# Optimization experiments

Measured on AMD Instinct MI355X. Metric: run time of the kernel, lower is better.

Reference implementation:

```python
import jax, jax.numpy as jnp
import numpy as np


def _grid_sample_bilinear(img, grid):
    # img: [N, C, H, W]; grid: [N, Ho, Wo, 2] (x,y) in [-1,1]
    # matches torch.nn.functional.grid_sample(mode='bilinear', padding_mode='zeros', align_corners=False)
    N, C, H, W = img.shape
    Ho, Wo = grid.shape[1], grid.shape[2]
    ix = (grid[..., 0] + 1.0) * (W * 0.5) - 0.5  # unnormalize, align_corners=False
    iy = (grid[..., 1] + 1.0) * (H * 0.5) - 0.5
    x0 = jnp.floor(ix)
    y0 = jnp.floor(iy)
    x1 = x0 + 1.0
    y1 = y0 + 1.0
    wx1 = ix - x0
    wx0 = 1.0 - wx1
    wy1 = iy - y0
    wy0 = 1.0 - wy1
    img_flat = img.reshape(N, C, H * W)

    def corner(xf, yf, w):
        valid = (xf >= 0) & (xf <= W - 1) & (yf >= 0) & (yf <= H - 1)
        xi = jnp.clip(xf.astype(jnp.int32), 0, W - 1)
        yi = jnp.clip(yf.astype(jnp.int32), 0, H - 1)
        idx = (yi * W + xi).reshape(N, 1, Ho * Wo)
        vals = jnp.take_along_axis(img_flat, idx, axis=2)  # [N, C, Ho*Wo]
        wv = (w * valid.astype(img.dtype)).reshape(N, 1, Ho * Wo)
        return vals * wv

    out = (corner(x0, y0, wx0 * wy0) + corner(x1, y0, wx1 * wy0)
           + corner(x0, y1, wx0 * wy1) + corner(x1, y1, wx1 * wy1))
    return out.reshape(N, C, Ho, Wo)


def setup_inputs() -> dict:
    key = jax.random.key(0)
    k1, k2 = jax.random.split(key)
    B, L, C, H, W = 2, 24, 16, 64, 64
    flows = jax.random.normal(k1, (B, L, 2, H, W), dtype=jnp.float32) * 0.01
    images = jax.random.normal(k2, (B, L, C, H, W), dtype=jnp.float32)
    return {"flows": flows, "images": images}


def reference(flows, images):
    B, L, _, H, W = flows.shape
    C = images.shape[2]
    dtype = flows.dtype
    cum_flows = jnp.cumsum(flows.astype(jnp.float32), axis=1).astype(dtype)  # [B,L,2,H,W]
    k_idx, t_idx = np.triu_indices(L)  # all pairs k <= t, N_pairs = L(L+1)/2
    N_pairs = k_idx.size
    # relative flow from frame k to frame t for every pair
    rel = (cum_flows[:, t_idx] - cum_flows[:, k_idx])  # [B, N_pairs, 2, H, W]
    rel = rel.reshape(B * N_pairs, 2, H, W).transpose(0, 2, 3, 1)  # [BN, H, W, 2]
    # pixel-center base grid (align_corners=False convention)
    gy = jnp.linspace(-1.0 + 1.0 / H, 1.0 - 1.0 / H, H, dtype=dtype)
    gx = jnp.linspace(-1.0 + 1.0 / W, 1.0 - 1.0 / W, W, dtype=dtype)
    base = jnp.stack(jnp.meshgrid(gx, gy, indexing='xy'), axis=-1)  # [H, W, 2] (x,y)
    grid = base[None] + rel
    # wrap x coordinate into [-1, 1)
    grid = grid.at[..., 0].set(jnp.remainder(grid[..., 0] + 1.0, 2.0) - 1.0)
    flat_images = images[:, k_idx].reshape(B * N_pairs, C, H, W)
    warped = _grid_sample_bilinear(flat_images, grid)  # [BN, C, H, W]
    targets = (np.arange(B)[:, None] * L + t_idx[None, :]).reshape(-1)
    out = jax.ops.segment_sum(warped, jnp.asarray(targets), num_segments=B * L)
    return out.reshape(B, L, C, H, W)
```

## Files before the change

kernel.cpp:

```cpp
#include <hip/hip_runtime.h>


#define BB 2
#define LL 24
#define CC 16
#define HH 64
#define WW 64
#define HW (HH * WW)

__device__ __forceinline__ void bilin_coords(
    float gxv0, float gyv,
    int& i00, int& i10, int& i01, int& i11,
    float& w00, float& w10, float& w01, float& w11)
{
    const float v = gxv0 + 1.0f;
    float r = v - 2.0f * truncf(v * 0.5f);
    r = (r < 0.0f) ? (r + 2.0f) : r;
    const float gxv = r - 1.0f;

    const float ix = (gxv + 1.0f) * 32.0f - 0.5f;
    const float iy = (gyv + 1.0f) * 32.0f - 0.5f;

    const float x0f = floorf(ix);
    const float y0f = floorf(iy);
    const float x1f = x0f + 1.0f;
    const float y1f = y0f + 1.0f;

    const float wx1 = ix - x0f, wx0 = 1.0f - wx1;
    const float wy1 = iy - y0f, wy0 = 1.0f - wy1;

    const bool vx0 = (x0f >= 0.0f) && (x0f <= 63.0f);
    const bool vx1 = (x1f >= 0.0f) && (x1f <= 63.0f);
    const bool vy0 = (y0f >= 0.0f) && (y0f <= 63.0f);
    const bool vy1 = (y1f >= 0.0f) && (y1f <= 63.0f);

    const int x0 = min(max((int)x0f, 0), WW - 1);
    const int x1 = min(max((int)x1f, 0), WW - 1);
    const int y0 = min(max((int)y0f, 0), HH - 1);
    const int y1 = min(max((int)y1f, 0), HH - 1);

    w00 = (vx0 && vy0) ? (wx0 * wy0) : 0.0f;
    w10 = (vx1 && vy0) ? (wx1 * wy0) : 0.0f;
    w01 = (vx0 && vy1) ? (wx0 * wy1) : 0.0f;
    w11 = (vx1 && vy1) ? (wx1 * wy1) : 0.0f;

    i00 = y0 * WW + x0;
    i10 = y0 * WW + x1;
    i01 = y1 * WW + x0;
    i11 = y1 * WW + x1;
}

__global__ __launch_bounds__(64) void transpose_kernel(
    const float* __restrict__ img, float* __restrict__ imgT)
{
    const int bid = blockIdx.x;
    const int y = bid % HH;
    const int l = (bid / HH) % LL;
    const int b = bid / (HH * LL);
    const int x = threadIdx.x;

    const float* src = img + ((size_t)(b * LL + l) * CC) * HW + y * WW + x;
    float v[CC];
#pragma unroll
    for (int c = 0; c < CC; ++c) v[c] = src[(size_t)c * HW];

    float* dst = imgT + ((size_t)(b * LL + l) * HW + y * WW + x) * CC;
#pragma unroll
    for (int c = 0; c < CC; c += 4)
        *(float4*)(dst + c) = make_float4(v[c], v[c + 1], v[c + 2], v[c + 3]);
}

__global__ __launch_bounds__(256) void gsps_main(
    const float* __restrict__ flows,
    const float* __restrict__ imgT,
    float* __restrict__ out)
{
    const int bid = blockIdx.x;
    const int t = (LL - 1) - (bid % LL);
    const int y = (bid / LL) % HH;
    const int b = bid / (LL * HH);
    const int x = threadIdx.x & 63;
    const int wave = threadIdx.x >> 6;
    const int cw = wave * 4;

    const float gx = -0.984375f + (float)x * 0.03125f;
    const float gy = -0.984375f + (float)y * 0.03125f;
    const int pix = y * WW + x;
    const float* fb = flows + (size_t)b * LL * 2 * HW + pix;

    float ctx = 0.0f, cty = 0.0f;
    for (int i = 0; i <= t; ++i) {
        ctx += fb[(size_t)(i * 2) * HW];
        cty += fb[(size_t)(i * 2 + 1) * HW];
    }

    float4 acc = make_float4(0.0f, 0.0f, 0.0f, 0.0f);
    float cx = 0.0f, cy = 0.0f;
    float fxk = fb[0];
    float fyk = fb[HW];

    const char* ibase = (const char*)(imgT + (size_t)b * LL * HW * CC) + cw * 4;

    for (int k = 0; k <= t; ++k) {
        cx += fxk; cy += fyk;

        if (k < t) {
            fxk = fb[(size_t)((k + 1) * 2) * HW];
            fyk = fb[(size_t)((k + 1) * 2 + 1) * HW];
        }

        int i00, i10, i01, i11;
        float w00, w10, w01, w11;
        bilin_coords(gx + (ctx - cx), gy + (cty - cy), i00, i10, i01, i11, w00, w10, w01, w11);

        const char* p = ibase + (size_t)k * (HW * CC * 4);
        const float4 v00 = *(const float4*)(p + (size_t)i00 * 64);
        const float4 v10 = *(const float4*)(p + (size_t)i10 * 64);
        const float4 v01 = *(const float4*)(p + (size_t)i01 * 64);
        const float4 v11 = *(const float4*)(p + (size_t)i11 * 64);

        acc.x += v00.x * w00 + v10.x * w10 + v01.x * w01 + v11.x * w11;
        acc.y += v00.y * w00 + v10.y * w10 + v01.y * w01 + v11.y * w11;
        acc.z += v00.z * w00 + v10.z * w10 + v01.z * w01 + v11.z * w11;
        acc.w += v00.w * w00 + v10.w * w10 + v01.w * w01 + v11.w * w11;
    }

    float* o = out + ((size_t)(b * LL + t) * CC + cw) * HW + pix;
    o[0]      = acc.x;
    o[HW]     = acc.y;
    o[2 * HW] = acc.z;
    o[3 * HW] = acc.w;
}

__global__ __launch_bounds__(256) void gsps_direct(
    const float* __restrict__ flows,
    const float* __restrict__ images,
    float* __restrict__ out)
{
    const int bid = blockIdx.x;
    const int t = (LL - 1) - (bid % LL);
    const int y = (bid / LL) % HH;
    const int b = bid / (LL * HH);
    const int x = threadIdx.x & 63;
    const int wave = threadIdx.x >> 6;
    const int cw = wave * 4;

    const float gx = -0.984375f + (float)x * 0.03125f;
    const float gy = -0.984375f + (float)y * 0.03125f;
    const int pix = y * WW + x;
    const float* fb = flows + (size_t)b * LL * 2 * HW + pix;

    float ctx = 0.0f, cty = 0.0f;
    for (int i = 0; i <= t; ++i) {
        ctx += fb[(size_t)(i * 2) * HW];
        cty += fb[(size_t)(i * 2 + 1) * HW];
    }

    float acc[4] = {0.0f, 0.0f, 0.0f, 0.0f};
    float cx = 0.0f, cy = 0.0f;
    float fxk = fb[0];
    float fyk = fb[HW];

    for (int k = 0; k <= t; ++k) {
        cx += fxk; cy += fyk;
        if (k < t) {
            fxk = fb[(size_t)((k + 1) * 2) * HW];
            fyk = fb[(size_t)((k + 1) * 2 + 1) * HW];
        }

        int i00, i10, i01, i11;
        float w00, w10, w01, w11;
        bilin_coords(gx + (ctx - cx), gy + (cty - cy), i00, i10, i01, i11, w00, w10, w01, w11);

        const float* img = images + (((size_t)(b * LL + k) * CC) + cw) * HW;
#pragma unroll
        for (int c = 0; c < 4; ++c) {
            const float* pc = img + (size_t)c * HW;
            acc[c] += pc[i00] * w00 + pc[i10] * w10 + pc[i01] * w01 + pc[i11] * w11;
        }
    }

    float* o = out + ((size_t)(b * LL + t) * CC + cw) * HW + pix;
#pragma unroll
    for (int c = 0; c < 4; ++c) o[(size_t)c * HW] = acc[c];
}

extern "C" void kernel_launch(void* const* d_in, const int* in_sizes, int n_in,
                              void* d_out, int out_size, void* d_ws, size_t ws_size,
                              hipStream_t stream) {
    const float* flows  = (const float*)d_in[0];
    const float* images = (const float*)d_in[1];
    float* out = (float*)d_out;

    const size_t needT = (size_t)BB * LL * CC * HW * sizeof(float);
    const int nblk = BB * LL * HH;

    if (ws_size >= needT) {
        float* imgT = (float*)d_ws;
        transpose_kernel<<<nblk, 64, 0, stream>>>(images, imgT);
        gsps_main<<<nblk, 256, 0, stream>>>(flows, imgT, out);
    } else {
        gsps_direct<<<nblk, 256, 0, stream>>>(flows, images, out);
    }
}
```

Before: 169.5 us.

## Compute all 16 channels per thread and interleave row-block order

```diff
diff --git a/kernel.cpp b/kernel.cpp
--- a/kernel.cpp
+++ b/kernel.cpp
@@ -70,9 +70,83 @@
         *(float4*)(dst + c) = make_float4(v[c], v[c + 1], v[c + 2], v[c + 3]);
 }
 
-__global__ __launch_bounds__(256) void gsps_main(
+__global__ __launch_bounds__(64) void gsps_main(
     const float* __restrict__ flows,
     const float* __restrict__ imgT,
+    float* __restrict__ out)
+{
+    const int bid = blockIdx.x;
+    const int y_lo = bid & 7;
+    const int r1 = bid >> 3;
+    const int t = (LL - 1) - (r1 % LL);
+    const int r2 = r1 / LL;
+    const int y = ((r2 & 7) << 3) | y_lo;
+    const int b = r2 >> 3;
+    const int x = threadIdx.x;
+
+    const float gx = -0.984375f + (float)x * 0.03125f;
+    const float gy = -0.984375f + (float)y * 0.03125f;
+    const int pix = y * WW + x;
+    const float* fb = flows + (size_t)b * LL * 2 * HW + pix;
+
+    float ctx = 0.0f, cty = 0.0f;
+    for (int i = 0; i <= t; ++i) {
+        ctx += fb[(size_t)(2 * i) * HW];
+        cty += fb[(size_t)(2 * i + 1) * HW];
+    }
+
+    float acc[CC];
+#pragma unroll
+    for (int c = 0; c < CC; ++c) acc[c] = 0.0f;
+
+    const char* pb = (const char*)imgT + (size_t)b * LL * HW * 64;
+    float cx = 0.0f, cy = 0.0f;
+    float fkx = fb[0], fky = fb[HW];
+
+    for (int k = 0; k <= t; ++k) {
+        cx += fkx; cy += fky;
+        if (k < t) {
+            fkx = fb[(size_t)(2 * (k + 1)) * HW];
+            fky = fb[(size_t)(2 * (k + 1) + 1) * HW];
+        }
+
+        int i00, i10, i01, i11;
+        float w00, w10, w01, w11;
+        bilin_coords(gx + (ctx - cx), gy + (cty - cy), i00, i10, i01, i11, w00, w10, w01, w11);
+
+        const char* plane = pb + (size_t)k * (HW * 64);
+        const float4* r00 = (const float4*)(plane + (size_t)i00 * 64);
+        const float4* r10 = (const float4*)(plane + (size_t)i10 * 64);
+        const float4* r01 = (const float4*)(plane + (size_t)i01 * 64);
+        const float4* r11 = (const float4*)(plane + (size_t)i11 * 64);
+
+        float4 v00[4], v10[4], v01[4], v11[4];
+#pragma unroll
+        for (int j = 0; j < 4; ++j) v00[j] = r00[j];
+#pragma unroll
+        for (int j = 0; j < 4; ++j) v10[j] = r10[j];
+#pragma unroll
+        for (int j = 0; j < 4; ++j) v01[j] = r01[j];
+#pragma unroll
+        for (int j = 0; j < 4; ++j) v11[j] = r11[j];
+
+#pragma unroll
+        for (int j = 0; j < 4; ++j) {
+            acc[4 * j + 0] += v00[j].x * w00 + v10[j].x * w10 + v01[j].x * w01 + v11[j].x * w11;
+            acc[4 * j + 1] += v00[j].y * w00 + v10[j].y * w10 + v01[j].y * w01 + v11[j].y * w11;
+            acc[4 * j + 2] += v00[j].z * w00 + v10[j].z * w10 + v01[j].z * w01 + v11[j].z * w11;
+            acc[4 * j + 3] += v00[j].w * w00 + v10[j].w * w10 + v01[j].w * w01 + v11[j].w * w11;
+        }
+    }
+
+    float* o = out + ((size_t)(b * LL + t) * CC) * HW + pix;
+#pragma unroll
+    for (int c = 0; c < CC; ++c) o[(size_t)c * HW] = acc[c];
+}
+
+__global__ __launch_bounds__(256) void gsps_direct(
+    const float* __restrict__ flows,
+    const float* __restrict__ images,
     float* __restrict__ out)
 {
     const int bid = blockIdx.x;
@@ -94,68 +168,6 @@
         cty += fb[(size_t)(i * 2 + 1) * HW];
     }
 
-    float4 acc = make_float4(0.0f, 0.0f, 0.0f, 0.0f);
-    float cx = 0.0f, cy = 0.0f;
-    float fxk = fb[0];
-    float fyk = fb[HW];
-
-    const char* ibase = (const char*)(imgT + (size_t)b * LL * HW * CC) + cw * 4;
-
-    for (int k = 0; k <= t; ++k) {
-        cx += fxk; cy += fyk;
-
-        if (k < t) {
-            fxk = fb[(size_t)((k + 1) * 2) * HW];
-            fyk = fb[(size_t)((k + 1) * 2 + 1) * HW];
-        }
-
-        int i00, i10, i01, i11;
-        float w00, w10, w01, w11;
-        bilin_coords(gx + (ctx - cx), gy + (cty - cy), i00, i10, i01, i11, w00, w10, w01, w11);
-
-        const char* p = ibase + (size_t)k * (HW * CC * 4);
-        const float4 v00 = *(const float4*)(p + (size_t)i00 * 64);
-        const float4 v10 = *(const float4*)(p + (size_t)i10 * 64);
-        const float4 v01 = *(const float4*)(p + (size_t)i01 * 64);
-        const float4 v11 = *(const float4*)(p + (size_t)i11 * 64);
-
-        acc.x += v00.x * w00 + v10.x * w10 + v01.x * w01 + v11.x * w11;
-        acc.y += v00.y * w00 + v10.y * w10 + v01.y * w01 + v11.y * w11;
-        acc.z += v00.z * w00 + v10.z * w10 + v01.z * w01 + v11.z * w11;
-        acc.w += v00.w * w00 + v10.w * w10 + v01.w * w01 + v11.w * w11;
-    }
-
-    float* o = out + ((size_t)(b * LL + t) * CC + cw) * HW + pix;
-    o[0]      = acc.x;
-    o[HW]     = acc.y;
-    o[2 * HW] = acc.z;
-    o[3 * HW] = acc.w;
-}
-
-__global__ __launch_bounds__(256) void gsps_direct(
-    const float* __restrict__ flows,
-    const float* __restrict__ images,
-    float* __restrict__ out)
-{
-    const int bid = blockIdx.x;
-    const int t = (LL - 1) - (bid % LL);
-    const int y = (bid / LL) % HH;
-    const int b = bid / (LL * HH);
-    const int x = threadIdx.x & 63;
-    const int wave = threadIdx.x >> 6;
-    const int cw = wave * 4;
-
-    const float gx = -0.984375f + (float)x * 0.03125f;
-    const float gy = -0.984375f + (float)y * 0.03125f;
-    const int pix = y * WW + x;
-    const float* fb = flows + (size_t)b * LL * 2 * HW + pix;
-
-    float ctx = 0.0f, cty = 0.0f;
-    for (int i = 0; i <= t; ++i) {
-        ctx += fb[(size_t)(i * 2) * HW];
-        cty += fb[(size_t)(i * 2 + 1) * HW];
-    }
-
     float acc[4] = {0.0f, 0.0f, 0.0f, 0.0f};
     float cx = 0.0f, cy = 0.0f;
     float fxk = fb[0];
@@ -198,7 +210,7 @@
     if (ws_size >= needT) {
         float* imgT = (float*)d_ws;
         transpose_kernel<<<nblk, 64, 0, stream>>>(images, imgT);
-        gsps_main<<<nblk, 256, 0, stream>>>(flows, imgT, out);
+        gsps_main<<<nblk, 64, 0, stream>>>(flows, imgT, out);
     } else {
         gsps_direct<<<nblk, 256, 0, stream>>>(flows, images, out);
     }
```

New measurement: 166.9 us. No clear change (-1.5%).
